# Kernel tuning notes

Hardware: AMD Instinct MI355X
Metric: run time of the kernel (lower is better)

## Reference

```python
import jax, jax.numpy as jnp
import numpy as np

C, NH, NW = 32, 64, 256  # channels, canvas height, canvas width (from __init__)
B, N = 64, 900_000       # batch size, number of voxels


def setup_inputs() -> dict:
    key = jax.random.key(0)
    kf, kp = jax.random.split(key)
    features = jax.random.normal(kf, (C, N), dtype=jnp.float32)
    # unique (b, h, w) cells -> no duplicate scatter indices (matches torch determinism)
    flat = jax.random.permutation(kp, B * NH * NW)[:N].astype(jnp.int32)
    b = flat // (NH * NW)
    rem = flat % (NH * NW)
    h = rem // NW
    w = rem % NW
    coords = jnp.stack([b, h, w], axis=1)  # [N, 3] int32
    return {"features": features, "coords": coords, "batch_size": B}


def reference(features, coords, batch_size):
    # features: [C, N]; coords: [N, 3] = (batch, h, w)
    # Single fused scatter over all batches: flatten (b, h, w) -> one index.
    flat_idx = coords[:, 0] * (NH * NW) + coords[:, 1] * NW + coords[:, 2]  # [N]
    canvas = jnp.zeros((batch_size * NH * NW, C), dtype=features.dtype)
    canvas = canvas.at[flat_idx].set(features.T)  # scatter voxel features
    # -> [B, C, NH, NW]
    return canvas.reshape(batch_size, NH, NW, C).transpose(0, 3, 1, 2)
```

## Files before the change

kernel.cpp:

```cpp
#include <hip/hip_runtime.h>

#define CC 32
#define BB 64
#define NHH 64
#define NWW 256
#define PLANE (NHH * NWW)
#define BSTRIDE (CC * PLANE)
#define NCELLS (BB * PLANE)
#define LROW 260

typedef float f32x4 __attribute__((ext_vector_type(4)));
typedef _Float16 f16x8 __attribute__((ext_vector_type(8)));

__global__ void pss_scatter_direct(const float* __restrict__ features,
                                   const int* __restrict__ coords,
                                   float* __restrict__ out, int N) {
    int n = blockIdx.x * blockDim.x + threadIdx.x;
    if (n >= N) return;
    int b = coords[3 * n + 0];
    int h = coords[3 * n + 1];
    int w = coords[3 * n + 2];
    int base = b * BSTRIDE + h * NWW + w;
#pragma unroll
    for (int c = 0; c < CC; ++c)
        out[base + c * PLANE] = features[c * N + n];
}

__global__ __launch_bounds__(256) void pss_zero(int4* __restrict__ p, int n4) {
    int i = blockIdx.x * blockDim.x + threadIdx.x;
    if (i < n4) p[i] = make_int4(0, 0, 0, 0);
}

__global__ __launch_bounds__(256) void pss_transpose_f16_dma(
        const float* __restrict__ features, const int* __restrict__ coords,
        f16x8* __restrict__ featT, int* __restrict__ invmap, int N) {
    __shared__ float lds[CC * LROW];

    int t = threadIdx.x;
    int lane = t & 63;
    int w = t >> 6;
    int n0 = blockIdx.x * 256;

    int n = n0 + t;
    if (n < N) {
        int b = coords[3 * n + 0];
        int h = coords[3 * n + 1];
        int ww = coords[3 * n + 2];
        invmap[b * PLANE + h * NWW + ww] = n + 1;
    }

    if (n0 + 256 <= N) {
#pragma unroll
        for (int r = 0; r < 8; ++r) {
            int c = 8 * w + r;
            const float* gp = &features[(size_t)c * N + n0 + 4 * lane];
            __builtin_amdgcn_global_load_lds(
                (const __attribute__((address_space(1))) void*)gp,
                (__attribute__((address_space(3))) void*)&lds[c * LROW],
                16, 0, 0);
        }
    } else {
#pragma unroll
        for (int r = 0; r < 8; ++r) {
            int c = 8 * w + r;
            int nn = n0 + 4 * lane;
            f32x4 v = (f32x4){0.f, 0.f, 0.f, 0.f};
            if (nn < N)
                v = *(const f32x4*)&features[(size_t)c * N + nn];
            *(f32x4*)&lds[c * LROW + 4 * lane] = v;
        }
    }

    __syncthreads();

#pragma unroll
    for (int j = 0; j < 4; ++j) {
        int idx = t + 256 * j;
        int nl = idx >> 2;
        int g = idx & 3;
        if (n0 + nl < N) {
            f16x8 hv;
#pragma unroll
            for (int e = 0; e < 8; ++e)
                hv[e] = (_Float16)lds[(8 * g + e) * LROW + nl];
            featT[(size_t)n0 * 4 + idx] = hv;
        }
    }
}

__global__ __launch_bounds__(256) void pss_gather_emit_f16(
        const f16x8* __restrict__ featT, const int* __restrict__ invmap,
        float* __restrict__ out) {
    __shared__ float lds[NWW * (CC + 1)];

    int row = blockIdx.x;
    int b = row / NHH;
    int h = row % NHH;
    int t = threadIdx.x;

    int inv = invmap[(size_t)row * NWW + t];

    if (inv > 0) {
        const f16x8* src = featT + (size_t)(inv - 1) * 4;
#pragma unroll
        for (int k = 0; k < 4; ++k) {
            f16x8 hv = src[k];
#pragma unroll
            for (int e = 0; e < 8; ++e)
                lds[t * (CC + 1) + 8 * k + e] = (float)hv[e];
        }
    } else {
#pragma unroll
        for (int k = 0; k < CC; ++k)
            lds[t * (CC + 1) + k] = 0.0f;
    }

    __syncthreads();

    size_t obase = (size_t)b * BSTRIDE + (size_t)h * NWW + t;
#pragma unroll
    for (int c = 0; c < CC; ++c) {
        float v = lds[t * (CC + 1) + c];
        __builtin_nontemporal_store(v, &out[obase + (size_t)c * PLANE]);
    }
}

extern "C" void kernel_launch(void* const* d_in, const int* in_sizes, int n_in,
                              void* d_out, int out_size, void* d_ws, size_t ws_size,
                              hipStream_t stream) {
    const float* features = (const float*)d_in[0];
    const int* coords = (const int*)d_in[1];
    float* out = (float*)d_out;
    const int N = in_sizes[1] / 3;

    const size_t invmap_bytes = (size_t)NCELLS * sizeof(int);
    const size_t featT_bytes = (size_t)N * CC * sizeof(_Float16);

    if (ws_size < invmap_bytes + featT_bytes) {
        (void)hipMemsetAsync(d_out, 0, (size_t)out_size * sizeof(float), stream);
        int blocks = (N + 255) / 256;
        pss_scatter_direct<<<blocks, 256, 0, stream>>>(features, coords, out, N);
        return;
    }

    int* invmap = (int*)d_ws;
    f16x8* featT = (f16x8*)((char*)d_ws + invmap_bytes);

    pss_zero<<<(NCELLS / 4 + 255) / 256, 256, 0, stream>>>((int4*)invmap,
                                                           NCELLS / 4);

    int tiles = (N + 255) / 256;
    pss_transpose_f16_dma<<<tiles, 256, 0, stream>>>(features, coords, featT,
                                                     invmap, N);

    pss_gather_emit_f16<<<BB * NHH, 256, 0, stream>>>(featT, invmap, out);
}
```

Before: 85.64 us.

## Split fp16 conversion from transpose into separate pass with f16 LDS transpose

Adds a grid-stride kernel that converts the channel-major fp32 features to fp16 in place-order and builds the inverse map. A second kernel then transposes the fp16 data in 512-voxel tiles through LDS, reading 32-bit pairs and repacking them into voxel-major fp16x8 vectors. The goal is a cheaper transpose stage with fewer LDS bytes and wider tiles. The cost is an extra workspace buffer, an extra full read and write pass over the features, and one more kernel launch.

Result: slower. 103.6 us (+21.0%).

```diff
diff --git a/kernel.cpp b/kernel.cpp
--- a/kernel.cpp
+++ b/kernel.cpp
@@ -7,7 +7,8 @@
 #define PLANE (NHH * NWW)
 #define BSTRIDE (CC * PLANE)
 #define NCELLS (BB * PLANE)
-#define LROW 260
+#define TN 512
+#define LSTR 520
 
 typedef float f32x4 __attribute__((ext_vector_type(4)));
 typedef _Float16 f16x8 __attribute__((ext_vector_type(8)));
@@ -31,43 +32,59 @@
     if (i < n4) p[i] = make_int4(0, 0, 0, 0);
 }
 
-__global__ __launch_bounds__(256) void pss_transpose_f16_dma(
+__global__ __launch_bounds__(256) void pss_convert_f16(
         const float* __restrict__ features, const int* __restrict__ coords,
-        f16x8* __restrict__ featT, int* __restrict__ invmap, int N) {
-    __shared__ float lds[CC * LROW];
+        f16x8* __restrict__ featC, int* __restrict__ invmap, int N, int units) {
+    const int nthreads = gridDim.x * 256;
+    const int gtid = blockIdx.x * 256 + threadIdx.x;
+
+    for (int n = gtid; n < N; n += nthreads) {
+        int b = coords[3 * n + 0];
+        int h = coords[3 * n + 1];
+        int w = coords[3 * n + 2];
+        invmap[b * PLANE + h * NWW + w] = n + 1;
+    }
+
+    for (int i = gtid; i < units; i += nthreads) {
+        const float* src = features + (size_t)i * 8;
+        f32x4 a = *(const f32x4*)src;
+        f32x4 b = *(const f32x4*)(src + 4);
+        f16x8 hv;
+        hv[0] = (_Float16)a.x; hv[1] = (_Float16)a.y;
+        hv[2] = (_Float16)a.z; hv[3] = (_Float16)a.w;
+        hv[4] = (_Float16)b.x; hv[5] = (_Float16)b.y;
+        hv[6] = (_Float16)b.z; hv[7] = (_Float16)b.w;
+        featC[i] = hv;
+    }
+}
+
+__global__ __launch_bounds__(256) void pss_transpose_f16f16(
+        const _Float16* __restrict__ featC, f16x8* __restrict__ featT, int N) {
+    __shared__ _Float16 lds16[CC * LSTR];
 
     int t = threadIdx.x;
     int lane = t & 63;
     int w = t >> 6;
-    int n0 = blockIdx.x * 256;
+    int n0 = blockIdx.x * TN;
 
-    int n = n0 + t;
-    if (n < N) {
-        int b = coords[3 * n + 0];
-        int h = coords[3 * n + 1];
-        int ww = coords[3 * n + 2];
-        invmap[b * PLANE + h * NWW + ww] = n + 1;
-    }
-
-    if (n0 + 256 <= N) {
+    if (n0 + TN <= N) {
 #pragma unroll
         for (int r = 0; r < 8; ++r) {
             int c = 8 * w + r;
-            const float* gp = &features[(size_t)c * N + n0 + 4 * lane];
+            const _Float16* gp = &featC[(size_t)c * N + n0 + 8 * lane];
             __builtin_amdgcn_global_load_lds(
                 (const __attribute__((address_space(1))) void*)gp,
-                (__attribute__((address_space(3))) void*)&lds[c * LROW],
+                (__attribute__((address_space(3))) void*)&lds16[c * LSTR],
                 16, 0, 0);
         }
     } else {
 #pragma unroll
         for (int r = 0; r < 8; ++r) {
             int c = 8 * w + r;
-            int nn = n0 + 4 * lane;
-            f32x4 v = (f32x4){0.f, 0.f, 0.f, 0.f};
-            if (nn < N)
-                v = *(const f32x4*)&features[(size_t)c * N + nn];
-            *(f32x4*)&lds[c * LROW + 4 * lane] = v;
+            int nn = n0 + 8 * lane;
+            f16x8 v = {};
+            if (nn < N) v = *(const f16x8*)&featC[(size_t)c * N + nn];
+            *(f16x8*)&lds16[c * LSTR + 8 * lane] = v;
         }
     }
 
@@ -75,15 +92,27 @@
 
 #pragma unroll
     for (int j = 0; j < 4; ++j) {
-        int idx = t + 256 * j;
-        int nl = idx >> 2;
-        int g = idx & 3;
-        if (n0 + nl < N) {
-            f16x8 hv;
+        int p = t + 256 * j;
+        int g = p & 3;
+        int nlp = p >> 2;
+        int nl0 = 2 * nlp;
+        if (n0 + nl0 < N) {
+            unsigned r[8];
 #pragma unroll
             for (int e = 0; e < 8; ++e)
-                hv[e] = (_Float16)lds[(8 * g + e) * LROW + nl];
-            featT[(size_t)n0 * 4 + idx] = hv;
+                r[e] = *(const unsigned*)&lds16[(8 * g + e) * LSTR + nl0];
+            unsigned lo[4], hi[4];
+#pragma unroll
+            for (int k = 0; k < 4; ++k) {
+                lo[k] = (r[2 * k] & 0xffffu) | (r[2 * k + 1] << 16);
+                hi[k] = (r[2 * k] >> 16) | (r[2 * k + 1] & 0xffff0000u);
+            }
+            unsigned* d0 = (unsigned*)&featT[((size_t)n0 + nl0) * 4 + g];
+            d0[0] = lo[0]; d0[1] = lo[1]; d0[2] = lo[2]; d0[3] = lo[3];
+            if (n0 + nl0 + 1 < N) {
+                unsigned* d1 = (unsigned*)&featT[((size_t)n0 + nl0 + 1) * 4 + g];
+                d1[0] = hi[0]; d1[1] = hi[1]; d1[2] = hi[2]; d1[3] = hi[3];
+            }
         }
     }
 }
@@ -134,9 +163,10 @@
     const int N = in_sizes[1] / 3;
 
     const size_t invmap_bytes = (size_t)NCELLS * sizeof(int);
-    const size_t featT_bytes = (size_t)N * CC * sizeof(_Float16);
+    const size_t featC_bytes = (size_t)N * CC * sizeof(_Float16);
+    const size_t featT_bytes = featC_bytes;
 
-    if (ws_size < invmap_bytes + featT_bytes) {
+    if (ws_size < invmap_bytes + featC_bytes + featT_bytes) {
         (void)hipMemsetAsync(d_out, 0, (size_t)out_size * sizeof(float), stream);
         int blocks = (N + 255) / 256;
         pss_scatter_direct<<<blocks, 256, 0, stream>>>(features, coords, out, N);
@@ -144,14 +174,18 @@
     }
 
     int* invmap = (int*)d_ws;
-    f16x8* featT = (f16x8*)((char*)d_ws + invmap_bytes);
+    _Float16* featC = (_Float16*)((char*)d_ws + invmap_bytes);
+    f16x8* featT = (f16x8*)((char*)d_ws + invmap_bytes + featC_bytes);
 
     pss_zero<<<(NCELLS / 4 + 255) / 256, 256, 0, stream>>>((int4*)invmap,
                                                            NCELLS / 4);
 
-    int tiles = (N + 255) / 256;
-    pss_transpose_f16_dma<<<tiles, 256, 0, stream>>>(features, coords, featT,
-                                                     invmap, N);
+    int units = (N * CC) / 8;
+    pss_convert_f16<<<2048, 256, 0, stream>>>(features, coords, (f16x8*)featC,
+                                              invmap, N, units);
+
+    int tiles = (N + TN - 1) / TN;
+    pss_transpose_f16f16<<<tiles, 256, 0, stream>>>(featC, featT, N);
 
     pss_gather_emit_f16<<<BB * NHH, 256, 0, stream>>>(featT, invmap, out);
 }
```

## Drop invmap zeroing via coords back-check validation; add XCD block swizzle

Applied to the files above, without the earlier changes.

Removes the separate kernel that zeroes the 4 MB inverse map. Each entry is now validated by checking the stored index is in range and that its coords map back to the same cell, so stale workspace contents are treated as empty. Both remaining kernels also remap block indices so consecutive tiles land on the same XCD, aiming for better L2 locality. The trade is an extra random coords read per occupied cell in the gather kernel.

New measurement: 94.91 us. 10.8% more time.

```diff
diff --git a/kernel.cpp b/kernel.cpp
--- a/kernel.cpp
+++ b/kernel.cpp
@@ -8,9 +8,16 @@
 #define BSTRIDE (CC * PLANE)
 #define NCELLS (BB * PLANE)
 #define LROW 260
+#define NXCD 8
 
 typedef float f32x4 __attribute__((ext_vector_type(4)));
 typedef _Float16 f16x8 __attribute__((ext_vector_type(8)));
+
+__device__ __forceinline__ int xcd_swizzle(int orig, int nwg) {
+    int q = nwg / NXCD, r = nwg % NXCD;
+    int xcd = orig % NXCD, pos = orig / NXCD;
+    return (xcd < r ? xcd * (q + 1) : r * (q + 1) + (xcd - r) * q) + pos;
+}
 
 __global__ void pss_scatter_direct(const float* __restrict__ features,
                                    const int* __restrict__ coords,
@@ -26,27 +33,23 @@
         out[base + c * PLANE] = features[c * N + n];
 }
 
-__global__ __launch_bounds__(256) void pss_zero(int4* __restrict__ p, int n4) {
-    int i = blockIdx.x * blockDim.x + threadIdx.x;
-    if (i < n4) p[i] = make_int4(0, 0, 0, 0);
-}
-
-__global__ __launch_bounds__(256) void pss_transpose_f16_dma(
+__global__ __launch_bounds__(256) void pss_transpose_f16_swz(
         const float* __restrict__ features, const int* __restrict__ coords,
-        f16x8* __restrict__ featT, int* __restrict__ invmap, int N) {
+        f16x8* __restrict__ featT, int* __restrict__ invmap, int N, int nwg) {
     __shared__ float lds[CC * LROW];
 
     int t = threadIdx.x;
     int lane = t & 63;
     int w = t >> 6;
-    int n0 = blockIdx.x * 256;
+    int tile = xcd_swizzle(blockIdx.x, nwg);
+    int n0 = tile * 256;
 
     int n = n0 + t;
     if (n < N) {
         int b = coords[3 * n + 0];
         int h = coords[3 * n + 1];
         int ww = coords[3 * n + 2];
-        invmap[b * PLANE + h * NWW + ww] = n + 1;
+        invmap[b * PLANE + h * NWW + ww] = n;
     }
 
     if (n0 + 256 <= N) {
@@ -88,20 +91,27 @@
     }
 }
 
-__global__ __launch_bounds__(256) void pss_gather_emit_f16(
+__global__ __launch_bounds__(256) void pss_gather_emit_v(
         const f16x8* __restrict__ featT, const int* __restrict__ invmap,
-        float* __restrict__ out) {
+        const int* __restrict__ coords, float* __restrict__ out, int N) {
     __shared__ float lds[NWW * (CC + 1)];
 
-    int row = blockIdx.x;
+    int row = xcd_swizzle(blockIdx.x, BB * NHH);
     int b = row / NHH;
     int h = row % NHH;
     int t = threadIdx.x;
 
-    int inv = invmap[(size_t)row * NWW + t];
+    int cell = row * NWW + t;
+    int inv = invmap[cell];
 
-    if (inv > 0) {
-        const f16x8* src = featT + (size_t)(inv - 1) * 4;
+    bool valid = ((unsigned)inv < (unsigned)N);
+    if (valid) {
+        valid = (coords[3 * inv + 0] * PLANE + coords[3 * inv + 1] * NWW +
+                 coords[3 * inv + 2]) == cell;
+    }
+
+    if (valid) {
+        const f16x8* src = featT + (size_t)inv * 4;
 #pragma unroll
         for (int k = 0; k < 4; ++k) {
             f16x8 hv = src[k];
@@ -146,12 +156,10 @@
     int* invmap = (int*)d_ws;
     f16x8* featT = (f16x8*)((char*)d_ws + invmap_bytes);
 
-    pss_zero<<<(NCELLS / 4 + 255) / 256, 256, 0, stream>>>((int4*)invmap,
-                                                           NCELLS / 4);
+    int tiles = (N + 255) / 256;
+    pss_transpose_f16_swz<<<tiles, 256, 0, stream>>>(features, coords, featT,
+                                                     invmap, N, tiles);
 
-    int tiles = (N + 255) / 256;
-    pss_transpose_f16_dma<<<tiles, 256, 0, stream>>>(features, coords, featT,
-                                                     invmap, N);
-
-    pss_gather_emit_f16<<<BB * NHH, 256, 0, stream>>>(featT, invmap, out);
+    pss_gather_emit_v<<<BB * NHH, 256, 0, stream>>>(featT, invmap, coords, out,
+                                                    N);
 }
```
